# Kernel tuning notes

Hardware: AMD Instinct MI355X
Metric: run time of the kernel (lower is better)

Reference implementation:

```python
import jax, jax.numpy as jnp
import numpy as np

D_MODEL = 1024
NUM_HEADS = 16
D_FF = 4096
B, T = 2, 2048
EPS = 1e-5


def setup_inputs() -> dict:
    key = jax.random.key(0)
    ks = jax.random.split(key, 8)
    s = 0.02
    return {
        "x": jax.random.normal(ks[0], (B, T, D_MODEL), dtype=jnp.float32),
        "wq": jax.random.normal(ks[1], (D_MODEL, D_MODEL), dtype=jnp.float32) * s,
        "wk": jax.random.normal(ks[2], (D_MODEL, D_MODEL), dtype=jnp.float32) * s,
        "wv": jax.random.normal(ks[3], (D_MODEL, D_MODEL), dtype=jnp.float32) * s,
        "wo": jax.random.normal(ks[4], (D_MODEL, D_MODEL), dtype=jnp.float32) * s,
        "w1": jax.random.normal(ks[5], (D_FF, D_MODEL), dtype=jnp.float32) * s,
        "w2": jax.random.normal(ks[6], (D_MODEL, D_FF), dtype=jnp.float32) * s,
        "g1": jnp.ones((D_MODEL,), dtype=jnp.float32),
        "g2": jnp.ones((D_MODEL,), dtype=jnp.float32),
    }


def rmsnorm(x, g):
    rms = jnp.sqrt(jnp.mean(x * x, axis=-1, keepdims=True) + EPS)
    return x / rms * g


def gelu(x):
    # exact erf-based GELU, as in the original module
    return 0.5 * x * (1.0 + jax.scipy.special.erf(x / jnp.sqrt(jnp.float32(2.0))))


def attention(x, wq, wk, wv, wo):
    b, t, d = x.shape
    d_k = d // NUM_HEADS
    # torch Linear: y = x @ W.T
    q = (x @ wq.T).reshape(b, t, NUM_HEADS, d_k).transpose(0, 2, 1, 3)
    k = (x @ wk.T).reshape(b, t, NUM_HEADS, d_k).transpose(0, 2, 1, 3)
    v = (x @ wv.T).reshape(b, t, NUM_HEADS, d_k).transpose(0, 2, 1, 3)
    scores = jnp.einsum("bhqd,bhkd->bhqk", q, k) / jnp.sqrt(jnp.float32(d_k))
    causal = jnp.triu(jnp.ones((t, t), dtype=bool), k=1)  # True above diagonal -> masked
    scores = jnp.where(causal, -jnp.inf, scores)
    attn = jax.nn.softmax(scores, axis=-1)
    out = jnp.einsum("bhqk,bhkd->bhqd", attn, v)
    out = out.transpose(0, 2, 1, 3).reshape(b, t, d)
    return out @ wo.T


def reference(x, wq, wk, wv, wo, w1, w2, g1, g2):
    x = x + attention(rmsnorm(x, g1), wq, wk, wv, wo)
    h = rmsnorm(x, g2)
    x = x + gelu(h @ w1.T) @ w2.T
    return x
```

## Files before the change

kernel.cpp:

```cpp
#include <hip/hip_runtime.h>
#include <stdint.h>

#define D_MODEL 1024
#define NUM_HEADS 16
#define D_FF 4096
#define BB 2
#define TT 2048
#define NROWS (BB * TT)

typedef __bf16 bf16x8 __attribute__((ext_vector_type(8)));
typedef short s16x8 __attribute__((ext_vector_type(8)));
typedef float f32x4 __attribute__((ext_vector_type(4)));

static __device__ __forceinline__ f32x4 mfma16(s16x8 a, s16x8 b, f32x4 c) {
  return __builtin_amdgcn_mfma_f32_16x16x32_bf16(
      __builtin_bit_cast(bf16x8, a), __builtin_bit_cast(bf16x8, b), c, 0, 0, 0);
}

static __device__ __forceinline__ short f2b(float f) {
  union { float f; uint32_t u; } v; v.f = f;
  return (short)((v.u + 0x7FFFu + ((v.u >> 16) & 1u)) >> 16);
}

typedef __attribute__((address_space(1))) const unsigned int gu32;
typedef __attribute__((address_space(3))) unsigned int lu32;
static __device__ __forceinline__ void gload16(const short* g, short* l) {
  __builtin_amdgcn_global_load_lds((gu32*)g, (lu32*)l, 16, 0, 0);
}

__global__ __launch_bounds__(256) void rmsnorm_kernel(
    const float* __restrict__ x, const float* __restrict__ g, short* __restrict__ out) {
  const int row = blockIdx.x;
  const int tid = threadIdx.x;
  const float4 xv = *(const float4*)(x + (size_t)row * D_MODEL + tid * 4);
  float ss = xv.x * xv.x + xv.y * xv.y + xv.z * xv.z + xv.w * xv.w;
#pragma unroll
  for (int off = 32; off >= 1; off >>= 1) ss += __shfl_down(ss, off);
  __shared__ float part[4];
  if ((tid & 63) == 0) part[tid >> 6] = ss;
  __syncthreads();
  const float tot = part[0] + part[1] + part[2] + part[3];
  const float sc = rsqrtf(tot * (1.0f / D_MODEL) + 1e-5f);
  const float4 gv = *(const float4*)(g + tid * 4);
  short4 o;
  o.x = f2b(xv.x * sc * gv.x);
  o.y = f2b(xv.y * sc * gv.y);
  o.z = f2b(xv.z * sc * gv.z);
  o.w = f2b(xv.w * sc * gv.w);
  *(short4*)(out + (size_t)row * D_MODEL + tid * 4) = o;
}

__global__ __launch_bounds__(256) void cvt_kernel(
    const float* __restrict__ in, short* __restrict__ out, int n) {
  const int i = (blockIdx.x * 256 + threadIdx.x) * 8;
  if (i >= n) return;
  const float4 a = *(const float4*)(in + i);
  const float4 b = *(const float4*)(in + i + 4);
  union { short s[8]; s16x8 v; } u;
  u.s[0] = f2b(a.x); u.s[1] = f2b(a.y); u.s[2] = f2b(a.z); u.s[3] = f2b(a.w);
  u.s[4] = f2b(b.x); u.s[5] = f2b(b.y); u.s[6] = f2b(b.z); u.s[7] = f2b(b.w);
  *(s16x8*)(out + i) = u.v;
}

__global__ __launch_bounds__(256) void cvt4_kernel(
    const float* __restrict__ a, const float* __restrict__ b,
    const float* __restrict__ c, const float* __restrict__ d,
    short* __restrict__ oa, short* __restrict__ ob,
    short* __restrict__ oc, short* __restrict__ od) {
  const int gid = blockIdx.x * 256 + threadIdx.x;
  const int seg = gid >> 17;
  const int off = (gid & 131071) * 8;
  const float* in = seg == 0 ? a : seg == 1 ? b : seg == 2 ? c : d;
  short* out = seg == 0 ? oa : seg == 1 ? ob : seg == 2 ? oc : od;
  const float4 lo = *(const float4*)(in + off);
  const float4 hi = *(const float4*)(in + off + 4);
  union { short s[8]; s16x8 v; } u;
  u.s[0] = f2b(lo.x); u.s[1] = f2b(lo.y); u.s[2] = f2b(lo.z); u.s[3] = f2b(lo.w);
  u.s[4] = f2b(hi.x); u.s[5] = f2b(hi.y); u.s[6] = f2b(hi.z); u.s[7] = f2b(hi.w);
  *(s16x8*)(out + off) = u.v;
}

template <int MFRAG>
__device__ __forceinline__ void gemm_core(
    const short* __restrict__ A, const short* __restrict__ Bw,
    int K, int brow, int bcol,
    short (&As)[2][MFRAG * 32][32], short (&Bs)[2][128][32],
    f32x4 (*acc)[4]) {
  const int tid = threadIdx.x;
  const int lane = tid & 63, wv = tid >> 6;
  const int l15 = lane & 15, lg = lane >> 4;
  const int wr = wv >> 1, wc = wv & 1;

  const int srow = wv * 16 + (lane >> 2);
  const int schunk = lane & 3;
  const short* Ag[MFRAG / 2];
  const short* Bg[2];
#pragma unroll
  for (int j = 0; j < MFRAG / 2; ++j)
    Ag[j] = A + (size_t)(brow + j * 64 + srow) * K + schunk * 8;
#pragma unroll
  for (int j = 0; j < 2; ++j)
    Bg[j] = Bw + (size_t)(bcol + j * 64 + srow) * K + schunk * 8;

#pragma unroll
  for (int j = 0; j < MFRAG / 2; ++j)
    gload16(Ag[j], &As[0][0][0] + j * 2048 + wv * 512);
#pragma unroll
  for (int j = 0; j < 2; ++j)
    gload16(Bg[j], &Bs[0][0][0] + j * 2048 + wv * 512);

  int cur = 0;
  for (int k0 = 0; k0 < K; k0 += 32) {
    __syncthreads();
    if (k0 + 32 < K) {
      const int nb = cur ^ 1, ko = k0 + 32;
#pragma unroll
      for (int j = 0; j < MFRAG / 2; ++j)
        gload16(Ag[j] + ko, &As[nb][0][0] + j * 2048 + wv * 512);
#pragma unroll
      for (int j = 0; j < 2; ++j)
        gload16(Bg[j] + ko, &Bs[nb][0][0] + j * 2048 + wv * 512);
    }
    s16x8 af[MFRAG], bfr[4];
#pragma unroll
    for (int m = 0; m < MFRAG; ++m)
      af[m] = *(const s16x8*)&As[cur][wr * (MFRAG * 16) + m * 16 + l15][lg * 8];
#pragma unroll
    for (int n = 0; n < 4; ++n)
      bfr[n] = *(const s16x8*)&Bs[cur][wc * 64 + n * 16 + l15][lg * 8];
#pragma unroll
    for (int m = 0; m < MFRAG; ++m)
#pragma unroll
      for (int n = 0; n < 4; ++n)
        acc[m][n] = mfma16(af[m], bfr[n], acc[m][n]);
    cur ^= 1;
  }
}

template <int MODE, int MFRAG>
__global__ __launch_bounds__(256) void gemm_bt(
    const short* __restrict__ A, const short* __restrict__ Bw,
    short* __restrict__ outb, float* __restrict__ outf,
    const float* __restrict__ resid, int K, int N) {
  __shared__ __align__(16) short As[2][MFRAG * 32][32];
  __shared__ __align__(16) short Bs[2][128][32];
  f32x4 acc[MFRAG][4] = {};
  const int brow = blockIdx.y * (MFRAG * 32), bcol = blockIdx.x * 128;
  gemm_core<MFRAG>(A, Bw, K, brow, bcol, As, Bs, acc);

  const int tid = threadIdx.x, lane = tid & 63;
  const int wv = tid >> 6, wr = wv >> 1, wc = wv & 1;
  const int l15 = lane & 15, lg = lane >> 4;
#pragma unroll
  for (int m = 0; m < MFRAG; ++m)
#pragma unroll
    for (int n = 0; n < 4; ++n)
#pragma unroll
      for (int r = 0; r < 4; ++r) {
        const int grow = brow + wr * (MFRAG * 16) + m * 16 + lg * 4 + r;
        const int gcol = bcol + wc * 64 + n * 16 + l15;
        const float v = acc[m][n][r];
        const size_t idx = (size_t)grow * N + gcol;
        if (MODE == 0) {
          outb[idx] = f2b(v);
        } else if (MODE == 2) {
          outf[idx] = v + resid[idx];
        } else {
          outb[idx] = f2b(0.5f * v * (1.0f + erff(v * 0.70710678118f)));
        }
      }
}

__global__ __launch_bounds__(256) void gemm_qkv(
    const short* __restrict__ A, const short* __restrict__ Wq,
    const short* __restrict__ Wk, const short* __restrict__ Wv,
    short* __restrict__ qout, short* __restrict__ kout, short* __restrict__ vtout) {
  __shared__ __align__(16) short As[2][128][32];
  __shared__ __align__(16) short Bs[2][128][32];
  const int sel = blockIdx.x >> 3;
  const int bcol = (blockIdx.x & 7) * 128;
  const int brow = blockIdx.y * 128;
  const short* Bw = sel == 0 ? Wq : sel == 1 ? Wk : Wv;
  f32x4 acc[4][4] = {};
  gemm_core<4>(A, Bw, 1024, brow, bcol, As, Bs, acc);

  const int tid = threadIdx.x, lane = tid & 63;
  const int wv = tid >> 6, wr = wv >> 1, wc = wv & 1;
  const int l15 = lane & 15, lg = lane >> 4;
  short* outb = sel == 0 ? qout : kout;
#pragma unroll
  for (int m = 0; m < 4; ++m)
#pragma unroll
    for (int n = 0; n < 4; ++n)
#pragma unroll
      for (int r = 0; r < 4; ++r) {
        const int grow = brow + wr * 64 + m * 16 + lg * 4 + r;
        const int gcol = bcol + wc * 64 + n * 16 + l15;
        float v = acc[m][n][r];
        if (sel == 0) v *= 0.125f;
        const short vb = f2b(v);
        if (sel < 2) {
          outb[(size_t)grow * 1024 + gcol] = vb;
        } else {
          const int bq = grow >> 11, t = grow & 2047;
          const int hh = gcol >> 6, d = gcol & 63;
          vtout[(((size_t)((bq << 4) + hh) << 6) + d) * 2048 + t] = vb;
        }
      }
}

__global__ __launch_bounds__(256) void attn_kernel(
    const short* __restrict__ qb, const short* __restrict__ kb,
    const short* __restrict__ vt, short* __restrict__ att) {
  const int bh = blockIdx.x, bq = bh >> 4, h = bh & 15;
  const int qbase = ((int)gridDim.y - 1 - (int)blockIdx.y) * 128;
  const int tid = threadIdx.x, lane = tid & 63, w = tid >> 6;
  const int l15 = lane & 15, lg = lane >> 4;

  __shared__ __align__(16) short Ks[2][64][64];
  __shared__ __align__(16) short Vs[2][64][64];
  __shared__ __align__(16) short Ps[4][32][64];

  const short* qhead = qb + (size_t)bq * 2048 * 1024 + h * 64;
  const short* khead = kb + (size_t)bq * 2048 * 1024 + h * 64;
  const short* vhead = vt + (size_t)bh * 64 * 2048;

  s16x8 aq[2][2];
#pragma unroll
  for (int mq = 0; mq < 2; ++mq) {
    const short* qp = qhead + (size_t)(qbase + mq * 64 + w * 16 + l15) * 1024 + lg * 8;
    aq[mq][0] = *(const s16x8*)(qp);
    aq[mq][1] = *(const s16x8*)(qp + 32);
  }

  f32x4 acc[2][4] = {};
  float mrow[2][4], lrow[2][4];
#pragma unroll
  for (int mq = 0; mq < 2; ++mq)
#pragma unroll
    for (int r = 0; r < 4; ++r) { mrow[mq][r] = -1e30f; lrow[mq][r] = 0.f; }

  const int ssub = lane >> 3;
  const int gch = (lane & 7) ^ ssub;
  const int swz = l15 & 7;

  const int nkt = qbase / 64 + 2;

#define STAGE_KV(buf, k0)                                                     \
  {                                                                           \
    _Pragma("unroll") for (int j = 0; j < 2; ++j) {                           \
      const int row = j * 32 + w * 8 + ssub;                                  \
      gload16(khead + (size_t)((k0) + row) * 1024 + gch * 8,                  \
              &Ks[buf][0][0] + j * 2048 + w * 512);                           \
      gload16(vhead + (size_t)row * 2048 + (k0) + gch * 8,                    \
              &Vs[buf][0][0] + j * 2048 + w * 512);                           \
    }                                                                         \
  }

  STAGE_KV(0, 0);
  int cur = 0;
  for (int kt = 0; kt < nkt; ++kt) {
    const int k0 = kt * 64;
    __syncthreads();
    if (kt + 1 < nkt) STAGE_KV(cur ^ 1, k0 + 64);

    const bool act0 = (k0 <= qbase + w * 16 + 15);

    s16x8 bk[4][2];
#pragma unroll
    for (int c = 0; c < 4; ++c) {
      const int r = c * 16 + l15;
#pragma unroll
      for (int kh = 0; kh < 2; ++kh)
        bk[c][kh] = *(const s16x8*)&Ks[cur][r][((kh * 4 + lg) ^ swz) * 8];
    }

    f32x4 s[2][4] = {};
    __builtin_amdgcn_s_setprio(1);
#pragma unroll
    for (int mq = 0; mq < 2; ++mq) {
      if (mq == 0 && !act0) continue;
#pragma unroll
      for (int c = 0; c < 4; ++c) {
        s[mq][c] = mfma16(aq[mq][0], bk[c][0], s[mq][c]);
        s[mq][c] = mfma16(aq[mq][1], bk[c][1], s[mq][c]);
      }
    }
    __builtin_amdgcn_s_setprio(0);

#pragma unroll
    for (int mq = 0; mq < 2; ++mq) {
      if (mq == 0 && !act0) continue;
      const int rbase = qbase + mq * 64 + w * 16;
      if (k0 + 63 > rbase) {
#pragma unroll
        for (int c = 0; c < 4; ++c) {
          const int kcol = k0 + c * 16 + l15;
#pragma unroll
          for (int r = 0; r < 4; ++r)
            if (kcol > rbase + lg * 4 + r) s[mq][c][r] = -1e30f;
        }
      }
      float mt[4];
#pragma unroll
      for (int r = 0; r < 4; ++r)
        mt[r] = fmaxf(fmaxf(s[mq][0][r], s[mq][1][r]), fmaxf(s[mq][2][r], s[mq][3][r]));
#pragma unroll
      for (int off = 8; off >= 1; off >>= 1)
#pragma unroll
        for (int r = 0; r < 4; ++r) mt[r] = fmaxf(mt[r], __shfl_xor(mt[r], off));
      bool need = false;
#pragma unroll
      for (int r = 0; r < 4; ++r) need = need || (mt[r] > mrow[mq][r] + 8.0f);
      if (__any(need)) {
#pragma unroll
        for (int r = 0; r < 4; ++r) {
          const float mnew = fmaxf(mrow[mq][r], mt[r]);
          const float scl = __expf(mrow[mq][r] - mnew);
          mrow[mq][r] = mnew;
          lrow[mq][r] *= scl;
#pragma unroll
          for (int df = 0; df < 4; ++df) acc[mq][df][r] *= scl;
        }
      }
#pragma unroll
      for (int c = 0; c < 4; ++c)
#pragma unroll
        for (int r = 0; r < 4; ++r) {
          const float p = __expf(s[mq][c][r] - mrow[mq][r]);
          lrow[mq][r] += p;
          const int prow = mq * 16 + lg * 4 + r;
          const int ch = c * 2 + (l15 >> 3);
          Ps[w][prow][((ch ^ (prow & 7)) << 3) + (l15 & 7)] = f2b(p);
        }
    }

    s16x8 bv[4][2];
#pragma unroll
    for (int df = 0; df < 4; ++df) {
      const int r = df * 16 + l15;
#pragma unroll
      for (int kh = 0; kh < 2; ++kh)
        bv[df][kh] = *(const s16x8*)&Vs[cur][r][((kh * 4 + lg) ^ swz) * 8];
    }

    __builtin_amdgcn_s_setprio(1);
#pragma unroll
    for (int mq = 0; mq < 2; ++mq) {
      if (mq == 0 && !act0) continue;
#pragma unroll
      for (int kh = 0; kh < 2; ++kh) {
        const s16x8 pa = *(const s16x8*)&Ps[w][mq * 16 + l15][((kh * 4 + lg) ^ swz) * 8];
#pragma unroll
        for (int df = 0; df < 4; ++df)
          acc[mq][df] = mfma16(pa, bv[df][kh], acc[mq][df]);
      }
    }
    __builtin_amdgcn_s_setprio(0);
    cur ^= 1;
  }

#pragma unroll
  for (int mq = 0; mq < 2; ++mq) {
#pragma unroll
    for (int off = 8; off >= 1; off >>= 1)
#pragma unroll
      for (int r = 0; r < 4; ++r) lrow[mq][r] += __shfl_xor(lrow[mq][r], off);
    float inv[4];
#pragma unroll
    for (int r = 0; r < 4; ++r) inv[r] = 1.0f / lrow[mq][r];
#pragma unroll
    for (int df = 0; df < 4; ++df)
#pragma unroll
      for (int r = 0; r < 4; ++r) {
        const int qrow = qbase + mq * 64 + w * 16 + lg * 4 + r;
        const int d = df * 16 + l15;
        att[((size_t)(bq * 2048) + qrow) * 1024 + h * 64 + d] =
            f2b(acc[mq][df][r] * inv[r]);
      }
  }
}

extern "C" void kernel_launch(void* const* d_in, const int* in_sizes, int n_in,
                              void* d_out, int out_size, void* d_ws, size_t ws_size,
                              hipStream_t stream) {
  const float* x  = (const float*)d_in[0];
  const float* wq = (const float*)d_in[1];
  const float* wk = (const float*)d_in[2];
  const float* wv = (const float*)d_in[3];
  const float* wo = (const float*)d_in[4];
  const float* w1 = (const float*)d_in[5];
  const float* w2 = (const float*)d_in[6];
  const float* g1 = (const float*)d_in[7];
  const float* g2 = (const float*)d_in[8];
  float* out = (float*)d_out;

  char* ws = (char*)d_ws;
  const size_t MB = 1u << 20;
  short* wq_b  = (short*)(ws + 0 * MB);
  short* wk_b  = (short*)(ws + 2 * MB);
  short* wv_b  = (short*)(ws + 4 * MB);
  short* wo_b  = (short*)(ws + 6 * MB);
  short* w1_b  = (short*)(ws + 8 * MB);
  short* w2_b  = (short*)(ws + 16 * MB);
  short* xn_b  = (short*)(ws + 24 * MB);
  short* q_b   = (short*)(ws + 32 * MB);
  short* k_b   = (short*)(ws + 40 * MB);
  short* vt_b  = (short*)(ws + 48 * MB);
  short* att_b = (short*)(ws + 56 * MB);
  short* gel_b = (short*)(ws + 32 * MB);

  rmsnorm_kernel<<<NROWS, 256, 0, stream>>>(x, g1, xn_b);
  cvt4_kernel<<<2048, 256, 0, stream>>>(wq, wk, wv, wo, wq_b, wk_b, wv_b, wo_b);
  cvt_kernel<<<2048, 256, 0, stream>>>(w1, w1_b, 1 << 22);
  cvt_kernel<<<2048, 256, 0, stream>>>(w2, w2_b, 1 << 22);
  gemm_qkv<<<dim3(24, 32), 256, 0, stream>>>(xn_b, wq_b, wk_b, wv_b, q_b, k_b, vt_b);
  attn_kernel<<<dim3(32, 16), 256, 0, stream>>>(q_b, k_b, vt_b, att_b);
  gemm_bt<2, 2><<<dim3(8, 64), 256, 0, stream>>>(att_b, wo_b, nullptr, out, x, 1024, 1024);
  rmsnorm_kernel<<<NROWS, 256, 0, stream>>>(out, g2, xn_b);
  gemm_bt<3, 4><<<dim3(32, 32), 256, 0, stream>>>(xn_b, w1_b, gel_b, nullptr, nullptr, 1024, 4096);
  gemm_bt<2, 2><<<dim3(8, 64), 256, 0, stream>>>(gel_b, w2_b, nullptr, out, out, 4096, 1024);
}
```

Before: 403.3 us.

## Swizzle GEMM LDS, split-K atomic FFN2, exp2 softmax, reorder attention blocks

Applies an XOR swizzle to GEMM shared-memory chunk placement so fragment reads avoid LDS bank conflicts. The second FFN GEMM now uses split-K over two slices with 128-row tiles and float atomic adds into the output, which already holds the residual. Softmax switches to exp2 with the log2(e) factor folded into the Q scale. The attention grid is flattened and ordered so heavy causal tiles launch first and light ones pair up. The atomics add contention and make the summation order nondeterministic.

New measurement: 406.2 us. About the same (+0.7%).

```diff
diff --git a/kernel.cpp b/kernel.cpp
--- a/kernel.cpp
+++ b/kernel.cpp
@@ -83,7 +83,7 @@
 template <int MFRAG>
 __device__ __forceinline__ void gemm_core(
     const short* __restrict__ A, const short* __restrict__ Bw,
-    int K, int brow, int bcol,
+    int Ksl, int lda, int ldb, int brow, int bcol,
     short (&As)[2][MFRAG * 32][32], short (&Bs)[2][128][32],
     f32x4 (*acc)[4]) {
   const int tid = threadIdx.x;
@@ -92,15 +92,16 @@
   const int wr = wv >> 1, wc = wv & 1;
 
   const int srow = wv * 16 + (lane >> 2);
-  const int schunk = lane & 3;
+  const int csrc = (lane & 3) ^ ((lane >> 3) & 3);
+  const int crd = (l15 >> 1) & 3;
   const short* Ag[MFRAG / 2];
   const short* Bg[2];
 #pragma unroll
   for (int j = 0; j < MFRAG / 2; ++j)
-    Ag[j] = A + (size_t)(brow + j * 64 + srow) * K + schunk * 8;
+    Ag[j] = A + (size_t)(brow + j * 64 + srow) * lda + csrc * 8;
 #pragma unroll
   for (int j = 0; j < 2; ++j)
-    Bg[j] = Bw + (size_t)(bcol + j * 64 + srow) * K + schunk * 8;
+    Bg[j] = Bw + (size_t)(bcol + j * 64 + srow) * ldb + csrc * 8;
 
 #pragma unroll
   for (int j = 0; j < MFRAG / 2; ++j)
@@ -110,9 +111,9 @@
     gload16(Bg[j], &Bs[0][0][0] + j * 2048 + wv * 512);
 
   int cur = 0;
-  for (int k0 = 0; k0 < K; k0 += 32) {
+  for (int k0 = 0; k0 < Ksl; k0 += 32) {
     __syncthreads();
-    if (k0 + 32 < K) {
+    if (k0 + 32 < Ksl) {
       const int nb = cur ^ 1, ko = k0 + 32;
 #pragma unroll
       for (int j = 0; j < MFRAG / 2; ++j)
@@ -124,10 +125,10 @@
     s16x8 af[MFRAG], bfr[4];
 #pragma unroll
     for (int m = 0; m < MFRAG; ++m)
-      af[m] = *(const s16x8*)&As[cur][wr * (MFRAG * 16) + m * 16 + l15][lg * 8];
+      af[m] = *(const s16x8*)&As[cur][wr * (MFRAG * 16) + m * 16 + l15][(lg ^ crd) * 8];
 #pragma unroll
     for (int n = 0; n < 4; ++n)
-      bfr[n] = *(const s16x8*)&Bs[cur][wc * 64 + n * 16 + l15][lg * 8];
+      bfr[n] = *(const s16x8*)&Bs[cur][wc * 64 + n * 16 + l15][(lg ^ crd) * 8];
 #pragma unroll
     for (int m = 0; m < MFRAG; ++m)
 #pragma unroll
@@ -141,12 +142,13 @@
 __global__ __launch_bounds__(256) void gemm_bt(
     const short* __restrict__ A, const short* __restrict__ Bw,
     short* __restrict__ outb, float* __restrict__ outf,
-    const float* __restrict__ resid, int K, int N) {
+    const float* __restrict__ resid, int Ksl, int lda, int N) {
   __shared__ __align__(16) short As[2][MFRAG * 32][32];
   __shared__ __align__(16) short Bs[2][128][32];
   f32x4 acc[MFRAG][4] = {};
   const int brow = blockIdx.y * (MFRAG * 32), bcol = blockIdx.x * 128;
-  gemm_core<MFRAG>(A, Bw, K, brow, bcol, As, Bs, acc);
+  const int kz = blockIdx.z * Ksl;
+  gemm_core<MFRAG>(A + kz, Bw + kz, Ksl, lda, lda, brow, bcol, As, Bs, acc);
 
   const int tid = threadIdx.x, lane = tid & 63;
   const int wv = tid >> 6, wr = wv >> 1, wc = wv & 1;
@@ -165,8 +167,10 @@
           outb[idx] = f2b(v);
         } else if (MODE == 2) {
           outf[idx] = v + resid[idx];
+        } else if (MODE == 3) {
+          outb[idx] = f2b(0.5f * v * (1.0f + erff(v * 0.70710678118f)));
         } else {
-          outb[idx] = f2b(0.5f * v * (1.0f + erff(v * 0.70710678118f)));
+          unsafeAtomicAdd(&outf[idx], v);
         }
       }
 }
@@ -182,7 +186,7 @@
   const int brow = blockIdx.y * 128;
   const short* Bw = sel == 0 ? Wq : sel == 1 ? Wk : Wv;
   f32x4 acc[4][4] = {};
-  gemm_core<4>(A, Bw, 1024, brow, bcol, As, Bs, acc);
+  gemm_core<4>(A, Bw, 1024, 1024, 1024, brow, bcol, As, Bs, acc);
 
   const int tid = threadIdx.x, lane = tid & 63;
   const int wv = tid >> 6, wr = wv >> 1, wc = wv & 1;
@@ -197,7 +201,7 @@
         const int grow = brow + wr * 64 + m * 16 + lg * 4 + r;
         const int gcol = bcol + wc * 64 + n * 16 + l15;
         float v = acc[m][n][r];
-        if (sel == 0) v *= 0.125f;
+        if (sel == 0) v *= 0.18033688011f;
         const short vb = f2b(v);
         if (sel < 2) {
           outb[(size_t)grow * 1024 + gcol] = vb;
@@ -210,10 +214,12 @@
 }
 
 __global__ __launch_bounds__(256) void attn_kernel(
-    const short* __restrict__ qb, const short* __restrict__ kb,
+    const short* __restrict__ qb_, const short* __restrict__ kb,
     const short* __restrict__ vt, short* __restrict__ att) {
-  const int bh = blockIdx.x, bq = bh >> 4, h = bh & 15;
-  const int qbase = ((int)gridDim.y - 1 - (int)blockIdx.y) * 128;
+  const int i = blockIdx.x;
+  const int bh = i & 31, bq = bh >> 4, h = bh & 15;
+  const int qtb = (i < 256) ? (15 - (i >> 5)) : ((i >> 5) - 8);
+  const int qbase = qtb * 128;
   const int tid = threadIdx.x, lane = tid & 63, w = tid >> 6;
   const int l15 = lane & 15, lg = lane >> 4;
 
@@ -221,7 +227,7 @@
   __shared__ __align__(16) short Vs[2][64][64];
   __shared__ __align__(16) short Ps[4][32][64];
 
-  const short* qhead = qb + (size_t)bq * 2048 * 1024 + h * 64;
+  const short* qhead = qb_ + (size_t)bq * 2048 * 1024 + h * 64;
   const short* khead = kb + (size_t)bq * 2048 * 1024 + h * 64;
   const short* vhead = vt + (size_t)bh * 64 * 2048;
 
@@ -316,7 +322,7 @@
 #pragma unroll
         for (int r = 0; r < 4; ++r) {
           const float mnew = fmaxf(mrow[mq][r], mt[r]);
-          const float scl = __expf(mrow[mq][r] - mnew);
+          const float scl = exp2f(mrow[mq][r] - mnew);
           mrow[mq][r] = mnew;
           lrow[mq][r] *= scl;
 #pragma unroll
@@ -327,7 +333,7 @@
       for (int c = 0; c < 4; ++c)
 #pragma unroll
         for (int r = 0; r < 4; ++r) {
-          const float p = __expf(s[mq][c][r] - mrow[mq][r]);
+          const float p = exp2f(s[mq][c][r] - mrow[mq][r]);
           lrow[mq][r] += p;
           const int prow = mq * 16 + lg * 4 + r;
           const int ch = c * 2 + (l15 >> 3);
@@ -415,9 +421,9 @@
   cvt_kernel<<<2048, 256, 0, stream>>>(w1, w1_b, 1 << 22);
   cvt_kernel<<<2048, 256, 0, stream>>>(w2, w2_b, 1 << 22);
   gemm_qkv<<<dim3(24, 32), 256, 0, stream>>>(xn_b, wq_b, wk_b, wv_b, q_b, k_b, vt_b);
-  attn_kernel<<<dim3(32, 16), 256, 0, stream>>>(q_b, k_b, vt_b, att_b);
-  gemm_bt<2, 2><<<dim3(8, 64), 256, 0, stream>>>(att_b, wo_b, nullptr, out, x, 1024, 1024);
+  attn_kernel<<<512, 256, 0, stream>>>(q_b, k_b, vt_b, att_b);
+  gemm_bt<2, 2><<<dim3(8, 64), 256, 0, stream>>>(att_b, wo_b, nullptr, out, x, 1024, 1024, 1024);
   rmsnorm_kernel<<<NROWS, 256, 0, stream>>>(out, g2, xn_b);
-  gemm_bt<3, 4><<<dim3(32, 32), 256, 0, stream>>>(xn_b, w1_b, gel_b, nullptr, nullptr, 1024, 4096);
-  gemm_bt<2, 2><<<dim3(8, 64), 256, 0, stream>>>(gel_b, w2_b, nullptr, out, out, 4096, 1024);
-}
+  gemm_bt<3, 4><<<dim3(32, 32), 256, 0, stream>>>(xn_b, w1_b, gel_b, nullptr, nullptr, 1024, 1024, 4096);
+  gemm_bt<4, 4><<<dim3(8, 32, 2), 256, 0, stream>>>(gel_b, w2_b, nullptr, out, nullptr, 2048, 4096, 1024);
+}
```
